# Optimization experiments

Hardware: AMD Instinct MI355X
Metric: run time of the kernel (lower is better)

## Reference

```python
import jax, jax.numpy as jnp
import numpy as np

T, B, OBS, H, A = 512, 64, 512, 1024, 18


def setup_inputs() -> dict:
    key = jax.random.key(0)
    ks = jax.random.split(key, 8)
    s = lambda fan: 1.0 / np.sqrt(fan)
    return {
        "obs": jax.random.normal(ks[0], (T, B, OBS), jnp.float32),
        # binary done/valid mask per (timestep, env)
        "mask": (jax.random.uniform(ks[1], (T, B)) > 0.05).astype(jnp.float32),
        "W_enc": jax.random.normal(ks[2], (H, OBS), jnp.float32) * s(OBS),
        "b_enc": jnp.zeros((H,), jnp.float32),
        "W_ih": jax.random.normal(ks[3], (4 * H, H), jnp.float32) * s(H),
        "b_ih": jnp.zeros((4 * H,), jnp.float32),
        "W_hh": jax.random.normal(ks[4], (4 * H, H), jnp.float32) * s(H),
        "b_hh": jnp.zeros((4 * H,), jnp.float32),
        "W_dec": jax.random.normal(ks[5], (A, H), jnp.float32) * s(H),
        "b_dec": jnp.zeros((A,), jnp.float32),
    }


def reference(obs, mask, W_enc, b_enc, W_ih, b_ih, W_hh, b_hh, W_dec, b_dec):
    # encoder MLP + relu, batched over all T*B (one big GEMM)
    encoded = jax.nn.relu(jnp.einsum("tbo,ho->tbh", obs, W_enc) + b_enc)
    # precompute input contribution to LSTM gates for all timesteps: [T,B,4H]
    x_gates = jnp.einsum("tbh,gh->tbg", encoded, W_ih) + b_ih + b_hh

    def step(carry, inp):
        h, c = carry
        xg, m = inp  # xg: [B,4H], m: [B]
        gates = xg + h @ W_hh.T
        i, f, g, o = jnp.split(gates, 4, axis=-1)  # torch LSTMCell order
        c_new = jax.nn.sigmoid(f) * c + jax.nn.sigmoid(i) * jnp.tanh(g)
        h_new = jax.nn.sigmoid(o) * jnp.tanh(c_new)
        m = m[:, None]
        h_new = h_new * m
        c_new = c_new * m
        return (h_new, c_new), h_new

    h0 = jnp.zeros((B, H), jnp.float32)
    c0 = jnp.zeros((B, H), jnp.float32)
    (h, c), latent = jax.lax.scan(step, (h0, c0), (x_gates, mask))

    # decoder over flattened (T*B, H) then mask q-values
    values = jnp.einsum("tbh,ah->tba", latent, W_dec) + b_dec
    values = values * mask[..., None]
    return values, h, c
```

## Files before the change

### kernel.cpp

```cpp
#include <hip/hip_runtime.h>
#include <hip/hip_bf16.h>

#define T_ 512
#define B_ 64
#define OBS_ 512
#define H_ 1024
#define A_ 18
#define MM_ (T_*B_)
#define G4_ (4*H_)
#define CH_ 64
#define NCH_ (T_/CH_)
#define CM_ (CH_*B_)

typedef unsigned short u16;
typedef unsigned long long u64;
typedef __attribute__((ext_vector_type(8))) short s8v;
typedef __attribute__((ext_vector_type(4))) float f4v;

__device__ __forceinline__ float b2f(u16 u){
    unsigned x = ((unsigned)u) << 16;
    return __builtin_bit_cast(float, x);
}
__device__ __forceinline__ u16 f2b(float f){
    unsigned x = __builtin_bit_cast(unsigned, f);
    return (u16)((x + 0x7fffu + ((x >> 16) & 1u)) >> 16);
}


__global__ void cast_f32_bf16(const float* __restrict__ in, u16* __restrict__ out, int n){
    int i = blockIdx.x * blockDim.x + threadIdx.x;
    int stride = gridDim.x * blockDim.x;
    for (; i < n; i += stride) out[i] = f2b(in[i]);
}

__global__ void add_bias2(const float* __restrict__ a, const float* __restrict__ b,
                          float* __restrict__ out, int n){
    int i = blockIdx.x * blockDim.x + threadIdx.x;
    if (i < n) out[i] = a[i] + b[i];
}

__global__ void init_scan(u16* __restrict__ h_hist, float* __restrict__ c,
                          unsigned* __restrict__ flags){
    int i = blockIdx.x * blockDim.x + threadIdx.x;
    int stride = gridDim.x * blockDim.x;
    unsigned* h0 = (unsigned*)h_hist;
    for (int k = i; k < B_*H_/2; k += stride) h0[k] = 0u;
    for (int k = i; k < B_*H_; k += stride) c[k] = 0.f;
    if (i < 512) flags[i] = 0u;
}

__global__ void copy_hc(const float* __restrict__ h, const float* __restrict__ c,
                        float* __restrict__ out){
    int i = blockIdx.x * blockDim.x + threadIdx.x;
    out[(size_t)MM_*A_ + i] = h[i];
    out[(size_t)MM_*A_ + B_*H_ + i] = c[i];
}


#define LDSS 72

template<bool A_FP32, bool RELU>
__global__ __launch_bounds__(256) void gemm_bt(
    const void* __restrict__ Aptr, const u16* __restrict__ W,
    const float* __restrict__ bias, u16* __restrict__ C,
    int M, int N, int K)
{
    __shared__ __align__(16) u16 As[128 * LDSS];
    __shared__ __align__(16) u16 Bs[128 * LDSS];

    const int tid  = threadIdx.x;
    const int lane = tid & 63;
    const int wid  = tid >> 6;
    const int wm   = wid & 1, wn = wid >> 1;
    const int m0   = blockIdx.y * 128, n0 = blockIdx.x * 128;
    const int quad = lane >> 4, l16 = lane & 15;

    f4v acc[4][4];
    #pragma unroll
    for (int i = 0; i < 4; i++)
        #pragma unroll
        for (int j = 0; j < 4; j++) acc[i][j] = (f4v){0.f,0.f,0.f,0.f};

    for (int k0 = 0; k0 < K; k0 += 64){
        __syncthreads();
        if (A_FP32){
            const float* A = (const float*)Aptr;
            #pragma unroll
            for (int pss = 0; pss < 8; pss++){
                int idx = pss * 256 + tid;
                int row = idx >> 4, ch = idx & 15;
                float4 v = *(const float4*)(A + (size_t)(m0 + row) * K + k0 + ch * 4);
                u16* d = &As[row * LDSS + ch * 4];
                d[0] = f2b(v.x); d[1] = f2b(v.y); d[2] = f2b(v.z); d[3] = f2b(v.w);
            }
        } else {
            const u16* A = (const u16*)Aptr;
            #pragma unroll
            for (int pss = 0; pss < 4; pss++){
                int idx = pss * 256 + tid;
                int row = idx >> 3, ch = idx & 7;
                *(uint4*)&As[row * LDSS + ch * 8] =
                    *(const uint4*)(A + (size_t)(m0 + row) * K + k0 + ch * 8);
            }
        }
        #pragma unroll
        for (int pss = 0; pss < 4; pss++){
            int idx = pss * 256 + tid;
            int row = idx >> 3, ch = idx & 7;
            *(uint4*)&Bs[row * LDSS + ch * 8] =
                *(const uint4*)(W + (size_t)(n0 + row) * K + k0 + ch * 8);
        }
        __syncthreads();

        #pragma unroll
        for (int kk = 0; kk < 64; kk += 32){
            s8v af[4], bf[4];
            #pragma unroll
            for (int mt = 0; mt < 4; mt++)
                af[mt] = *(const s8v*)&As[(wm*64 + mt*16 + l16) * LDSS + kk + quad*8];
            #pragma unroll
            for (int nt = 0; nt < 4; nt++)
                bf[nt] = *(const s8v*)&Bs[(wn*64 + nt*16 + l16) * LDSS + kk + quad*8];
            #pragma unroll
            for (int mt = 0; mt < 4; mt++)
                #pragma unroll
                for (int nt = 0; nt < 4; nt++)
                    acc[mt][nt] = __builtin_amdgcn_mfma_f32_16x16x32_bf16(
                        af[mt], bf[nt], acc[mt][nt], 0, 0, 0);
        }
    }

    #pragma unroll
    for (int mt = 0; mt < 4; mt++){
        #pragma unroll
        for (int nt = 0; nt < 4; nt++){
            #pragma unroll
            for (int r = 0; r < 4; r++){
                int m = m0 + wm*64 + mt*16 + quad*4 + r;
                int n = n0 + wn*64 + nt*16 + l16;
                float v = acc[mt][nt][r] + bias[n];
                if (RELU) v = fmaxf(v, 0.f);
                C[(size_t)m * N + n] = f2b(v);
            }
        }
    }
}


__global__ __launch_bounds__(256, 1) void lstm_scan(
    const u16* __restrict__ xg,
    const u16* __restrict__ Whh,
    u16* __restrict__ h_hist,
    float* __restrict__ c_glob,
    float* __restrict__ h_f32,
    const float* __restrict__ mask,
    unsigned* __restrict__ flags,
    int t0)
{
    __shared__ float red[4][4][16][17];

    const int tid  = threadIdx.x;
    const int lane = tid & 63;
    const int w    = tid >> 6;
    const int quad = lane >> 4, l16 = lane & 15;
    const int bid  = blockIdx.x;
    const int g = bid & 3, s = bid >> 2;
    const int rb0 = g * 16, j0 = s * 16;

    const int koff = w * 256;
    s8v bf[4][8];
    #pragma unroll
    for (int gate = 0; gate < 4; gate++)
        #pragma unroll
        for (int ks = 0; ks < 8; ks++)
            bf[gate][ks] = *(const s8v*)(
                Whh + (size_t)(gate * H_ + j0 + l16) * H_ + koff + ks * 32 + quad * 8);

    const int cb = tid >> 4, cu = tid & 15;
    const size_t cidx = (size_t)(rb0 + cb) * H_ + j0 + cu;
    float c_reg = c_glob[cidx];

    const size_t hoff = (size_t)(rb0 + l16) * H_ + koff + quad * 8;

    unsigned* myflag = flags + ((g * 4 + (s >> 4)) << 5) + (s & 15);
    const unsigned* pollp = flags + ((g * 4 + w) << 5) + l16;

    const u16* xg0 = xg + (size_t)(rb0 + cb) * G4_ + j0 + cu;
    u16 nxi = xg0[0], nxf = xg0[H_], nxv = xg0[2 * H_], nxo = xg0[3 * H_];
    float nm = mask[rb0 + cb];

    for (int st = 0; st < CH_; st++){
        const float xi = b2f(nxi), xf = b2f(nxf), xv = b2f(nxv), xo = b2f(nxo);
        const float m = nm;

        const unsigned tgt = (unsigned)(t0 + st);
        int tries = 0;
        for (;;){
            unsigned f = __hip_atomic_load(pollp, __ATOMIC_RELAXED, __HIP_MEMORY_SCOPE_AGENT);
            if (__all((int)(f >= tgt))) break;
            if (++tries > (1 << 20)) break;
            if (tries >= 8) __builtin_amdgcn_s_sleep(1);
        }

        const u16* hs = h_hist + (size_t)st * B_ * H_ + hoff;
        f4v acc[4];
        #pragma unroll
        for (int gate = 0; gate < 4; gate++) acc[gate] = (f4v){0.f,0.f,0.f,0.f};
        #pragma unroll
        for (int ks = 0; ks < 8; ks++){
            s8v af = *(const s8v*)(hs + ks * 32);
            #pragma unroll
            for (int gate = 0; gate < 4; gate++)
                acc[gate] = __builtin_amdgcn_mfma_f32_16x16x32_bf16(af, bf[gate][ks], acc[gate], 0, 0, 0);
        }
        #pragma unroll
        for (int gate = 0; gate < 4; gate++)
            #pragma unroll
            for (int r = 0; r < 4; r++)
                red[w][gate][quad * 4 + r][l16] = acc[gate][r];
        __syncthreads();

        float gi = xi, gf = xf, gg = xv, go = xo;
        #pragma unroll
        for (int ww = 0; ww < 4; ww++){
            gi += red[ww][0][cb][cu];
            gf += red[ww][1][cb][cu];
            gg += red[ww][2][cb][cu];
            go += red[ww][3][cb][cu];
        }

        float is = 1.f / (1.f + __expf(-gi));
        float fs = 1.f / (1.f + __expf(-gf));
        float os = 1.f / (1.f + __expf(-go));
        float gt = tanhf(gg);

        float cn = fs * c_reg + is * gt;
        float hn = os * tanhf(cn);
        hn *= m; cn *= m;
        c_reg = cn;
        if (t0 + st == T_ - 1) h_f32[cidx] = hn;

        unsigned hb = (unsigned)f2b(hn);
        unsigned partner = (unsigned)__shfl_xor((int)hb, 1, 64);
        if ((cu & 1) == 0){
            unsigned packed = hb | (partner << 16);
            unsigned* dst = (unsigned*)(h_hist + (size_t)(st + 1) * B_ * H_ + cidx);
            __hip_atomic_store(dst, packed, __ATOMIC_RELAXED, __HIP_MEMORY_SCOPE_AGENT);
            if (st == CH_ - 1){
                unsigned* dst0 = (unsigned*)(h_hist + cidx);
                __hip_atomic_store(dst0, packed, __ATOMIC_RELAXED, __HIP_MEMORY_SCOPE_AGENT);
            }
        }
        asm volatile("s_waitcnt vmcnt(0)" ::: "memory");
        __syncthreads();

        if (tid == 0)
            __hip_atomic_store(myflag, (unsigned)(t0 + st + 1),
                               __ATOMIC_RELAXED, __HIP_MEMORY_SCOPE_AGENT);

        if (st + 1 < CH_){
            const u16* xgn = xg + (size_t)(st + 1) * B_ * G4_ + (size_t)(rb0 + cb) * G4_ + j0 + cu;
            nxi = xgn[0]; nxf = xgn[H_]; nxv = xgn[2 * H_]; nxo = xgn[3 * H_];
            nm = mask[(size_t)(st + 1) * B_ + rb0 + cb];
        }
    }

    c_glob[cidx] = c_reg;
}


__global__ __launch_bounds__(256) void decode_kernel(
    const u16* __restrict__ latent, const u16* __restrict__ Wdec,
    const float* __restrict__ bdec, const float* __restrict__ mask,
    float* __restrict__ values, int rows)
{
    __shared__ __align__(16) u16 wl[A_ * H_];
    const int tid = threadIdx.x;
    for (int i = tid; i < A_ * H_ / 8; i += 256)
        ((uint4*)wl)[i] = ((const uint4*)Wdec)[i];
    __syncthreads();

    const int lane = tid & 63;
    int wid = blockIdx.x * 4 + (tid >> 6);
    const int nwaves = gridDim.x * 4;

    for (int row = wid; row < rows; row += nwaves){
        float lat[16];
        #pragma unroll
        for (int i = 0; i < 16; i++)
            lat[i] = b2f(latent[(size_t)row * H_ + i*64 + lane]);
        float acc[A_];
        #pragma unroll
        for (int a = 0; a < A_; a++) acc[a] = 0.f;
        #pragma unroll
        for (int i = 0; i < 16; i++){
            #pragma unroll
            for (int a = 0; a < A_; a++)
                acc[a] += lat[i] * b2f(wl[a * H_ + i*64 + lane]);
        }
        float m = mask[row];
        #pragma unroll
        for (int a = 0; a < A_; a++){
            float v = acc[a];
            #pragma unroll
            for (int s = 32; s > 0; s >>= 1) v += __shfl_down(v, s, 64);
            if (lane == 0) values[(size_t)row * A_ + a] = (v + bdec[a]) * m;
        }
    }
}


extern "C" void kernel_launch(void* const* d_in, const int* in_sizes, int n_in,
                              void* d_out, int out_size, void* d_ws, size_t ws_size,
                              hipStream_t stream)
{
    const float* obs  = (const float*)d_in[0];
    const float* mask = (const float*)d_in[1];
    const float* Wenc = (const float*)d_in[2];
    const float* benc = (const float*)d_in[3];
    const float* Wih  = (const float*)d_in[4];
    const float* bih  = (const float*)d_in[5];
    const float* Whh  = (const float*)d_in[6];
    const float* bhh  = (const float*)d_in[7];
    const float* Wdec = (const float*)d_in[8];
    const float* bdec = (const float*)d_in[9];
    float* out = (float*)d_out;

    char* p = (char*)d_ws;
    size_t o = 0;
    auto alloc = [&](size_t bytes){ void* r = p + o; o += (bytes + 255) & ~(size_t)255; return r; };
    u16*      wenc_b  = (u16*)     alloc((size_t)H_ * OBS_ * 2);
    u16*      wih_b   = (u16*)     alloc((size_t)G4_ * H_ * 2);
    u16*      whh_b   = (u16*)     alloc((size_t)G4_ * H_ * 2);
    u16*      wdec_b  = (u16*)     alloc((size_t)A_ * H_ * 2);
    float*    bias2   = (float*)   alloc((size_t)G4_ * 4);
    u16*      enc_ch  = (u16*)     alloc((size_t)CM_ * H_ * 2);
    u16*      xg_ch   = (u16*)     alloc((size_t)CM_ * G4_ * 2);
    u16*      h_hist  = (u16*)     alloc((size_t)(CH_ + 1) * B_ * H_ * 2);
    float*    h_f32   = (float*)   alloc((size_t)B_ * H_ * 4);
    float*    c_f32   = (float*)   alloc((size_t)B_ * H_ * 4);
    unsigned* flags   = (unsigned*)alloc(512 * 4);
    (void)ws_size; (void)in_sizes; (void)n_in; (void)out_size;

    cast_f32_bf16<<<1024, 256, 0, stream>>>(Wenc, wenc_b, H_ * OBS_);
    cast_f32_bf16<<<2048, 256, 0, stream>>>(Wih,  wih_b,  G4_ * H_);
    cast_f32_bf16<<<2048, 256, 0, stream>>>(Whh,  whh_b,  G4_ * H_);
    cast_f32_bf16<<<72,   256, 0, stream>>>(Wdec, wdec_b, A_ * H_);
    add_bias2<<<16, 256, 0, stream>>>(bih, bhh, bias2, G4_);
    init_scan<<<2048, 256, 0, stream>>>(h_hist, c_f32, flags);

    for (int c = 0; c < NCH_; c++){
        const int t0 = c * CH_;

        dim3 g1(H_ / 128, CM_ / 128);
        gemm_bt<true, true><<<g1, 256, 0, stream>>>(
            obs + (size_t)t0 * B_ * OBS_, wenc_b, benc, enc_ch, CM_, H_, OBS_);

        dim3 g2(G4_ / 128, CM_ / 128);
        gemm_bt<false, false><<<g2, 256, 0, stream>>>(
            enc_ch, wih_b, bias2, xg_ch, CM_, G4_, H_);

        lstm_scan<<<256, 256, 0, stream>>>(
            xg_ch, whh_b, h_hist, c_f32, h_f32,
            mask + (size_t)t0 * B_, flags, t0);

        decode_kernel<<<256, 256, 0, stream>>>(
            h_hist + (size_t)B_ * H_, wdec_b, bdec, mask + (size_t)t0 * B_,
            out + (size_t)t0 * B_ * A_, CM_);
    }

    copy_hc<<<256, 256, 0, stream>>>(h_f32, c_f32, out);
}
```

Baseline: 2.630 ms.

## Overlap next chunk's input-gate GEMM with LSTM scan in one fused launch

The LSTM scan kernel gains 256 extra blocks that compute the next chunk's x-gate GEMM while the 256 scan blocks run the recurrence. The encoder GEMM runs once over all timesteps, and the x-gates are double-buffered across chunks. The aim is to hide the serial per-chunk GEMM time behind the latency-bound scan. The catch is that the GEMM blocks compete for CUs and memory bandwidth with the scan blocks, which depend on persistent co-residency and flag-based sync. The path is used only when the workspace is large enough, and falls back to the old per-chunk launches otherwise.

```diff
diff --git a/kernel.cpp b/kernel.cpp
--- a/kernel.cpp
+++ b/kernel.cpp
@@ -11,6 +11,7 @@
 #define CH_ 64
 #define NCH_ (T_/CH_)
 #define CM_ (CH_*B_)
+#define NG_ 256
 
 typedef unsigned short u16;
 typedef unsigned long long u64;
@@ -147,7 +148,7 @@
 }
 
 
-__global__ __launch_bounds__(256, 1) void lstm_scan(
+__global__ __launch_bounds__(256, 1) void fused_scan_gemm(
     const u16* __restrict__ xg,
     const u16* __restrict__ Whh,
     u16* __restrict__ h_hist,
@@ -155,14 +156,86 @@
     float* __restrict__ h_f32,
     const float* __restrict__ mask,
     unsigned* __restrict__ flags,
-    int t0)
+    int t0,
+    const u16* __restrict__ encA,
+    const u16* __restrict__ Wih,
+    const float* __restrict__ bias2,
+    u16* __restrict__ xg_next,
+    int ntiles)
 {
-    __shared__ float red[4][4][16][17];
+    __shared__ __align__(16) char smem[2 * 128 * LDSS * 2];
 
     const int tid  = threadIdx.x;
     const int lane = tid & 63;
     const int w    = tid >> 6;
     const int quad = lane >> 4, l16 = lane & 15;
+
+    if (blockIdx.x >= 256){
+        if (ntiles == 0) return;
+        u16* As = (u16*)smem;
+        u16* Bs = As + 128 * LDSS;
+        const int wm = w & 1, wn = w >> 1;
+
+        for (int tile = (int)blockIdx.x - 256; tile < ntiles; tile += NG_){
+            const int n0 = (tile & 31) * 128;
+            const int m0 = (tile >> 5) * 128;
+
+            f4v acc[4][4];
+            #pragma unroll
+            for (int i = 0; i < 4; i++)
+                #pragma unroll
+                for (int j = 0; j < 4; j++) acc[i][j] = (f4v){0.f,0.f,0.f,0.f};
+
+            for (int k0 = 0; k0 < H_; k0 += 64){
+                __syncthreads();
+                #pragma unroll
+                for (int pss = 0; pss < 4; pss++){
+                    int idx = pss * 256 + tid;
+                    int row = idx >> 3, ch = idx & 7;
+                    *(uint4*)&As[row * LDSS + ch * 8] =
+                        *(const uint4*)(encA + (size_t)(m0 + row) * H_ + k0 + ch * 8);
+                    *(uint4*)&Bs[row * LDSS + ch * 8] =
+                        *(const uint4*)(Wih + (size_t)(n0 + row) * H_ + k0 + ch * 8);
+                }
+                __syncthreads();
+
+                #pragma unroll
+                for (int kk = 0; kk < 64; kk += 32){
+                    s8v af[4], bf[4];
+                    #pragma unroll
+                    for (int mt = 0; mt < 4; mt++)
+                        af[mt] = *(const s8v*)&As[(wm*64 + mt*16 + l16) * LDSS + kk + quad*8];
+                    #pragma unroll
+                    for (int nt = 0; nt < 4; nt++)
+                        bf[nt] = *(const s8v*)&Bs[(wn*64 + nt*16 + l16) * LDSS + kk + quad*8];
+                    #pragma unroll
+                    for (int mt = 0; mt < 4; mt++)
+                        #pragma unroll
+                        for (int nt = 0; nt < 4; nt++)
+                            acc[mt][nt] = __builtin_amdgcn_mfma_f32_16x16x32_bf16(
+                                af[mt], bf[nt], acc[mt][nt], 0, 0, 0);
+                }
+            }
+            __syncthreads();
+
+            #pragma unroll
+            for (int mt = 0; mt < 4; mt++){
+                #pragma unroll
+                for (int nt = 0; nt < 4; nt++){
+                    #pragma unroll
+                    for (int r = 0; r < 4; r++){
+                        int m = m0 + wm*64 + mt*16 + quad*4 + r;
+                        int n = n0 + wn*64 + nt*16 + l16;
+                        xg_next[(size_t)m * G4_ + n] = f2b(acc[mt][nt][r] + bias2[n]);
+                    }
+                }
+            }
+        }
+        return;
+    }
+
+    float (*red)[4][16][17] = (float(*)[4][16][17])smem;
+
     const int bid  = blockIdx.x;
     const int g = bid & 3, s = bid >> 2;
     const int rb0 = g * 16, j0 = s * 16;
@@ -334,13 +407,15 @@
     u16*      whh_b   = (u16*)     alloc((size_t)G4_ * H_ * 2);
     u16*      wdec_b  = (u16*)     alloc((size_t)A_ * H_ * 2);
     float*    bias2   = (float*)   alloc((size_t)G4_ * 4);
-    u16*      enc_ch  = (u16*)     alloc((size_t)CM_ * H_ * 2);
-    u16*      xg_ch   = (u16*)     alloc((size_t)CM_ * G4_ * 2);
     u16*      h_hist  = (u16*)     alloc((size_t)(CH_ + 1) * B_ * H_ * 2);
     float*    h_f32   = (float*)   alloc((size_t)B_ * H_ * 4);
     float*    c_f32   = (float*)   alloc((size_t)B_ * H_ * 4);
     unsigned* flags   = (unsigned*)alloc(512 * 4);
-    (void)ws_size; (void)in_sizes; (void)n_in; (void)out_size;
+
+    const size_t enc_all_b = (size_t)MM_ * H_ * 2;
+    const size_t xg_b      = (size_t)CM_ * G4_ * 2;
+    const bool big = ws_size >= o + enc_all_b + 2 * xg_b + 4096;
+    (void)in_sizes; (void)n_in; (void)out_size;
 
     cast_f32_bf16<<<1024, 256, 0, stream>>>(Wenc, wenc_b, H_ * OBS_);
     cast_f32_bf16<<<2048, 256, 0, stream>>>(Wih,  wih_b,  G4_ * H_);
@@ -349,24 +424,57 @@
     add_bias2<<<16, 256, 0, stream>>>(bih, bhh, bias2, G4_);
     init_scan<<<2048, 256, 0, stream>>>(h_hist, c_f32, flags);
 
-    for (int c = 0; c < NCH_; c++){
-        const int t0 = c * CH_;
-
-        dim3 g1(H_ / 128, CM_ / 128);
-        gemm_bt<true, true><<<g1, 256, 0, stream>>>(
-            obs + (size_t)t0 * B_ * OBS_, wenc_b, benc, enc_ch, CM_, H_, OBS_);
-
-        dim3 g2(G4_ / 128, CM_ / 128);
-        gemm_bt<false, false><<<g2, 256, 0, stream>>>(
-            enc_ch, wih_b, bias2, xg_ch, CM_, G4_, H_);
-
-        lstm_scan<<<256, 256, 0, stream>>>(
-            xg_ch, whh_b, h_hist, c_f32, h_f32,
-            mask + (size_t)t0 * B_, flags, t0);
-
-        decode_kernel<<<256, 256, 0, stream>>>(
-            h_hist + (size_t)B_ * H_, wdec_b, bdec, mask + (size_t)t0 * B_,
-            out + (size_t)t0 * B_ * A_, CM_);
+    if (big){
+        u16* enc_all = (u16*)alloc(enc_all_b);
+        u16* xg_buf0 = (u16*)alloc(xg_b);
+        u16* xg_buf1 = (u16*)alloc(xg_b);
+        u16* xg_buf[2] = { xg_buf0, xg_buf1 };
+
+        dim3 ge(H_ / 128, MM_ / 128);
+        gemm_bt<true, true><<<ge, 256, 0, stream>>>(
+            obs, wenc_b, benc, enc_all, MM_, H_, OBS_);
+
+        dim3 gx(G4_ / 128, CM_ / 128);
+        gemm_bt<false, false><<<gx, 256, 0, stream>>>(
+            enc_all, wih_b, bias2, xg_buf[0], CM_, G4_, H_);
+
+        for (int c = 0; c < NCH_; c++){
+            const int t0 = c * CH_;
+            const int nt = (c + 1 < NCH_) ? 1024 : 0;
+            fused_scan_gemm<<<256 + NG_, 256, 0, stream>>>(
+                xg_buf[c & 1], whh_b, h_hist, c_f32, h_f32,
+                mask + (size_t)t0 * B_, flags, t0,
+                enc_all + (size_t)(c + 1) * CM_ * H_, wih_b, bias2,
+                xg_buf[(c + 1) & 1], nt);
+
+            decode_kernel<<<256, 256, 0, stream>>>(
+                h_hist + (size_t)B_ * H_, wdec_b, bdec, mask + (size_t)t0 * B_,
+                out + (size_t)t0 * B_ * A_, CM_);
+        }
+    } else {
+        u16* enc_ch = (u16*)alloc((size_t)CM_ * H_ * 2);
+        u16* xg_ch  = (u16*)alloc(xg_b);
+
+        for (int c = 0; c < NCH_; c++){
+            const int t0 = c * CH_;
+
+            dim3 g1(H_ / 128, CM_ / 128);
+            gemm_bt<true, true><<<g1, 256, 0, stream>>>(
+                obs + (size_t)t0 * B_ * OBS_, wenc_b, benc, enc_ch, CM_, H_, OBS_);
+
+            dim3 g2(G4_ / 128, CM_ / 128);
+            gemm_bt<false, false><<<g2, 256, 0, stream>>>(
+                enc_ch, wih_b, bias2, xg_ch, CM_, G4_, H_);
+
+            fused_scan_gemm<<<256, 256, 0, stream>>>(
+                xg_ch, whh_b, h_hist, c_f32, h_f32,
+                mask + (size_t)t0 * B_, flags, t0,
+                (const u16*)nullptr, wih_b, bias2, (u16*)nullptr, 0);
+
+            decode_kernel<<<256, 256, 0, stream>>>(
+                h_hist + (size_t)B_ * H_, wdec_b, bdec, mask + (size_t)t0 * B_,
+                out + (size_t)t0 * B_ * A_, CM_);
+        }
     }
 
     copy_hc<<<256, 256, 0, stream>>>(h_f32, c_f32, out);
```

Result: slower. 2.736 ms (+4.0%).
